# Performance work log

Measured on AMD Instinct MI355X. Metric: run time of the kernel, lower is better.

## Reference

```python
import jax, jax.numpy as jnp
import numpy as np

HEIGHT = 32
SIGMA = 2.0
NUM_NEGATIVE = 4096
N, C = 32, 512
L = HEIGHT * HEIGHT


def _grid_weight(height: int, sigma: float) -> jnp.ndarray:
    # distance_weights: pairwise Euclidean distance between grid points
    ii, jj = np.meshgrid(np.arange(height), np.arange(height), indexing='ij')
    coords = np.stack([ii.ravel(), jj.ravel()], axis=1).astype(np.float32)  # [L, 2]
    d2 = ((coords[:, None, :] - coords[None, :, :]) ** 2).sum(-1)  # squared dist [L, L]
    w = -(0.5 / sigma ** 2) * d2
    np.fill_diagonal(w, -np.inf)
    return jax.nn.softmax(jnp.asarray(w, dtype=jnp.float32), axis=1)


def setup_inputs() -> dict:
    key = jax.random.key(0)
    k1, k2 = jax.random.split(key)
    embedding = jax.random.normal(k1, (N, L, C), dtype=jnp.float32)
    weight = _grid_weight(HEIGHT, SIGMA)  # [L, L] softmax-normalized grid kernel
    neg_indices = jax.random.randint(k2, (NUM_NEGATIVE,), 0, N * L, dtype=jnp.int64)
    return {"embedding": embedding, "weight": weight, "neg_indices": neg_indices}


def reference(embedding, weight, neg_indices):
    n, l, c = embedding.shape
    # F.normalize(dim=-1), eps=1e-12
    norm = jnp.maximum(jnp.linalg.norm(embedding, axis=-1, keepdims=True), 1e-12)
    e = embedding / norm  # [N, L, C]
    # target = weight @ e  (broadcast over batch)
    target = jnp.einsum('kl,nlc->nkc', weight, e)  # [N, L, C]
    sim_pos = jnp.sum(e * target, axis=-1)  # [N, L]
    flat = e.reshape(-1, c)  # [N*L, C]
    negatives = flat[neg_indices]  # [M, C]
    sim_neg = jnp.einsum('nlc,mc->nlm', e, negatives)  # [N, L, M]
    logits = jnp.concatenate([sim_pos[..., None], sim_neg], axis=2).reshape(n * l, 1 + neg_indices.shape[0])
    # CrossEntropyLoss with target class 0, mean reduction
    loss = -jnp.mean(jax.nn.log_softmax(logits, axis=-1)[:, 0])
    return loss
```

## Files before the change

### kernel.cpp

```cpp
#include <hip/hip_runtime.h>
#include <hip/hip_bf16.h>
#include <stdint.h>

#define L_DIM 1024
#define C_DIM 512
#define CB4 256
#define N_BATCH 32
#define M_NEG 4096
#define NROWS (N_BATCH * L_DIM)

typedef float f32x4 __attribute__((ext_vector_type(4)));
typedef int i32x4 __attribute__((ext_vector_type(4)));
typedef int i32x8 __attribute__((ext_vector_type(8)));

#define E4_SCALE 32.0f
#define MX_SCALE 122
#define FMT_FP4 4

__device__ __forceinline__ void gl_lds16(const uint8_t* g, uint8_t* l) {
  __builtin_amdgcn_global_load_lds(
      (const __attribute__((address_space(1))) void*)g,
      (__attribute__((address_space(3))) void*)l, 16, 0, 0);
}

__device__ __forceinline__ uint32_t fp4_enc(float x) {
  const uint32_t s = (__float_as_uint(x) >> 31) << 3;
  const float a = fabsf(x);
  uint32_t c;
  c = a < 0.25f ? 0u
    : a < 0.75f ? 1u
    : a < 1.25f ? 2u
    : a < 1.75f ? 3u
    : a < 2.5f  ? 4u
    : a < 3.5f  ? 5u
    : a < 5.0f  ? 6u : 7u;
  return s | c;
}

__global__ __launch_bounds__(256) void k_normalize(const float* __restrict__ emb,
                                                   uint8_t* __restrict__ out,
                                                   float* __restrict__ zerobuf) {
  if (blockIdx.x < 256) zerobuf[blockIdx.x * 256 + threadIdx.x] = 0.0f;
  const int lane = threadIdx.x & 63;
  const int wave = threadIdx.x >> 6;
  const long row = (long)blockIdx.x * 4 + wave;
  const float4* src = (const float4*)(emb + row * C_DIM);
  float4 v0 = src[2 * lane];
  float4 v1 = src[2 * lane + 1];
  float ss = v0.x * v0.x + v0.y * v0.y + v0.z * v0.z + v0.w * v0.w +
             v1.x * v1.x + v1.y * v1.y + v1.z * v1.z + v1.w * v1.w;
#pragma unroll
  for (int off = 1; off < 64; off <<= 1) ss += __shfl_xor(ss, off, 64);
  const float s = E4_SCALE / fmaxf(sqrtf(ss), 1e-12f);
  uint32_t pk = fp4_enc(v0.x * s)        | (fp4_enc(v0.y * s) << 4) |
                (fp4_enc(v0.z * s) << 8) | (fp4_enc(v0.w * s) << 12) |
                (fp4_enc(v1.x * s) << 16)| (fp4_enc(v1.y * s) << 20) |
                (fp4_enc(v1.z * s) << 24)| (fp4_enc(v1.w * s) << 28);
  ((uint32_t*)(out + row * CB4))[lane] = pk;
}

__global__ __launch_bounds__(256, 2) void k_gemm_fused(
    const uint8_t* __restrict__ E4, const int* __restrict__ idx,
    const float* __restrict__ W, float* __restrict__ rowsum,
    float* __restrict__ simpos) {
  __shared__ __align__(16) unsigned char smem_raw[40960];
  uint8_t* sA = (uint8_t*)smem_raw;
  uint8_t* sB = sA + 256 * 64;

  const int tid = threadIdx.x;
  const int lane = tid & 63;
  const int wave = tid >> 6;
  const int wm = wave >> 1, wn = wave & 1;
  const int q = lane >> 4, c16 = lane & 15;

  const int bid = blockIdx.x;
  const bool is0 = bid >= 1024;
  long rowBase, colBase, n = 0;
  if (is0) {
    const int t = bid - 1024;
    const int xcd = t & 7, slot = t >> 3;
    rowBase = (long)(xcd * 16 + (slot & 15)) * 256;
    colBase = (long)(slot >> 4) * 128;
  } else {
    const int xcd = bid & 7, slot = bid >> 3;
    n = xcd * 4 + (slot & 3);
    const int inner = slot >> 2;
    rowBase = (long)(inner & 3) * 256;
    colBase = (long)(inner >> 2) * 128;
  }
  const long aBase = is0 ? rowBase : n * L_DIM + rowBase;

  long offA[4], offB[2];
#pragma unroll
  for (int r = 0; r < 4; ++r) {
    const int c = r * 256 + tid;
    const int rw = c >> 2, cb = c & 3;
    offA[r] = (aBase + rw) * CB4 + (cb ^ (rw & 3)) * 16;
  }
#pragma unroll
  for (int r = 0; r < 2; ++r) {
    const int c = r * 256 + tid;
    const int rw = c >> 2, cb = c & 3;
    const long bRow = is0 ? (long)idx[colBase + rw] : n * L_DIM + colBase + rw;
    offB[r] = bRow * CB4 + (cb ^ (rw & 3)) * 16;
  }

  f32x4 acc[8][4] = {};
  const i32x4 zz = {0, 0, 0, 0};

#pragma unroll
  for (int ks = 0; ks < CB4; ks += 64) {
#pragma unroll
    for (int r = 0; r < 4; ++r)
      gl_lds16(E4 + offA[r] + ks, sA + (r * 256 + tid) * 16);
#pragma unroll
    for (int r = 0; r < 2; ++r)
      gl_lds16(E4 + offB[r] + ks, sB + (r * 256 + tid) * 16);
    __syncthreads();
    i32x8 bfr[4];
#pragma unroll
    for (int j = 0; j < 4; ++j) {
      const int row = wn * 64 + j * 16 + c16;
      i32x4 d = *(const i32x4*)(sB + row * 64 + (q ^ (row & 3)) * 16);
      bfr[j] = __builtin_shufflevector(d, zz, 0, 1, 2, 3, 4, 5, 6, 7);
    }
#pragma unroll
    for (int i = 0; i < 8; ++i) {
      const int row = wm * 128 + i * 16 + c16;
      i32x4 d = *(const i32x4*)(sA + row * 64 + (q ^ (row & 3)) * 16);
      i32x8 af = __builtin_shufflevector(d, zz, 0, 1, 2, 3, 4, 5, 6, 7);
#pragma unroll
      for (int j = 0; j < 4; ++j)
        acc[i][j] = __builtin_amdgcn_mfma_scale_f32_16x16x128_f8f6f4(
            af, bfr[j], acc[i][j], FMT_FP4, FMT_FP4,
            0, MX_SCALE, 0, MX_SCALE);
    }
    __syncthreads();
  }

  if (is0) {
    float* S = (float*)smem_raw;
#pragma unroll
    for (int i = 0; i < 8; ++i)
#pragma unroll
      for (int r = 0; r < 4; ++r) {
        const float s = __expf(acc[i][0][r]) + __expf(acc[i][1][r]) +
                        __expf(acc[i][2][r]) + __expf(acc[i][3][r]);
        S[wave * 2560 + (i * 16 + q * 4 + r) * 20 + c16] = s;
      }
    __syncthreads();
    {
      const int wmg = tid >> 7, rs = tid & 127;
      const float4* p0 = (const float4*)(S + (wmg * 2 + 0) * 2560 + rs * 20);
      const float4* p1 = (const float4*)(S + (wmg * 2 + 1) * 2560 + rs * 20);
      float4 t0 = p0[0], t1 = p0[1], t2 = p0[2], t3 = p0[3];
      float4 u0 = p1[0], u1 = p1[1], u2 = p1[2], u3 = p1[3];
      float v = t0.x + t0.y + t0.z + t0.w + t1.x + t1.y + t1.z + t1.w +
                t2.x + t2.y + t2.z + t2.w + t3.x + t3.y + t3.z + t3.w +
                u0.x + u0.y + u0.z + u0.w + u1.x + u1.y + u1.z + u1.w +
                u2.x + u2.y + u2.z + u2.w + u3.x + u3.y + u3.z + u3.w;
      atomicAdd(&rowsum[rowBase + tid], v);
    }
  } else {
    float* G = (float*)smem_raw;
#pragma unroll
    for (int p = 0; p < 4; ++p) {
      if (wm == (p >> 1)) {
        const int ib = (p & 1) * 4;
#pragma unroll
        for (int ii = 0; ii < 4; ++ii)
#pragma unroll
          for (int j = 0; j < 4; ++j)
#pragma unroll
            for (int r = 0; r < 4; ++r)
              G[(ii * 16 + q * 4 + r) * 132 + wn * 64 + j * 16 + c16] =
                  acc[ib + ii][j][r];
      }
      __syncthreads();
      {
        const int rr = tid >> 2;
        const int chunk = tid & 3;
        const long krow = rowBase + p * 64 + rr;
        float v = 0.0f;
#pragma unroll
        for (int u = 0; u < 8; ++u) {
          const float4 g = *(const float4*)(G + rr * 132 + u * 16 + chunk * 4);
          const float4 w4 =
              *(const float4*)(W + krow * L_DIM + colBase + u * 16 + chunk * 4);
          v += g.x * w4.x + g.y * w4.y + g.z * w4.z + g.w * w4.w;
        }
        v += __shfl_xor(v, 1, 64);
        v += __shfl_xor(v, 2, 64);
        if (chunk == 0) atomicAdd(&simpos[n * L_DIM + krow], v);
      }
      __syncthreads();
    }
  }
}

__global__ __launch_bounds__(1024) void k_finalize(const float* __restrict__ rowsum,
                                                   const float* __restrict__ simpos,
                                                   float* __restrict__ out) {
  const int tid = threadIdx.x;
  float local = 0.0f;
  for (int r = tid; r < NROWS; r += 1024) {
    const float sp = simpos[r];
    local += logf(rowsum[r] + __expf(sp)) - sp;
  }
#pragma unroll
  for (int off = 1; off < 64; off <<= 1) local += __shfl_xor(local, off, 64);
  __shared__ float ws[16];
  if ((tid & 63) == 0) ws[tid >> 6] = local;
  __syncthreads();
  if (tid < 64) {
    float v = (tid < 16) ? ws[tid] : 0.0f;
#pragma unroll
    for (int off = 1; off < 16; off <<= 1) v += __shfl_xor(v, off, 64);
    if (tid == 0) out[0] = v * (1.0f / (float)NROWS);
  }
}

extern "C" void kernel_launch(void* const* d_in, const int* in_sizes, int n_in,
                              void* d_out, int out_size, void* d_ws, size_t ws_size,
                              hipStream_t stream) {
  const float* emb = (const float*)d_in[0];
  const float* weight = (const float*)d_in[1];
  const int* negidx = (const int*)d_in[2];
  float* out = (float*)d_out;
  char* ws = (char*)d_ws;

  uint8_t* E4 = (uint8_t*)ws;
  float* rowsum = (float*)(ws + 8388608);
  float* simpos = (float*)(ws + 8519680);

  k_normalize<<<NROWS / 4, 256, 0, stream>>>(emb, E4, rowsum);
  k_gemm_fused<<<5120, 256, 0, stream>>>(E4, negidx, weight, rowsum, simpos);
  k_finalize<<<1, 1024, 0, stream>>>(rowsum, simpos, out);
}
```

Before: 177.2 us.

## Load GEMM fragments directly from global memory and parallelize finalize reduction

The fused GEMM now loads FP4 MFMA operand fragments from global memory straight into registers instead of staging tiles through LDS with barriers. This removes LDS writes and reads and all syncthreads in the K loop, at the cost of redundant global reads across waves and strided, less coalesced access. The finalize kernel becomes a multi-block grid that reduces per block and atomically accumulates into the output, which is now zeroed in the normalize kernel. This replaces the single-block serial reduction.

```diff
diff --git a/kernel.cpp b/kernel.cpp
--- a/kernel.cpp
+++ b/kernel.cpp
@@ -16,12 +16,6 @@
 #define E4_SCALE 32.0f
 #define MX_SCALE 122
 #define FMT_FP4 4
-
-__device__ __forceinline__ void gl_lds16(const uint8_t* g, uint8_t* l) {
-  __builtin_amdgcn_global_load_lds(
-      (const __attribute__((address_space(1))) void*)g,
-      (__attribute__((address_space(3))) void*)l, 16, 0, 0);
-}
 
 __device__ __forceinline__ uint32_t fp4_enc(float x) {
   const uint32_t s = (__float_as_uint(x) >> 31) << 3;
@@ -39,8 +33,10 @@
 
 __global__ __launch_bounds__(256) void k_normalize(const float* __restrict__ emb,
                                                    uint8_t* __restrict__ out,
-                                                   float* __restrict__ zerobuf) {
+                                                   float* __restrict__ zerobuf,
+                                                   float* __restrict__ loss_out) {
   if (blockIdx.x < 256) zerobuf[blockIdx.x * 256 + threadIdx.x] = 0.0f;
+  if (blockIdx.x == 0 && threadIdx.x == 0) loss_out[0] = 0.0f;
   const int lane = threadIdx.x & 63;
   const int wave = threadIdx.x >> 6;
   const long row = (long)blockIdx.x * 4 + wave;
@@ -64,8 +60,6 @@
     const float* __restrict__ W, float* __restrict__ rowsum,
     float* __restrict__ simpos) {
   __shared__ __align__(16) unsigned char smem_raw[40960];
-  uint8_t* sA = (uint8_t*)smem_raw;
-  uint8_t* sB = sA + 256 * 64;
 
   const int tid = threadIdx.x;
   const int lane = tid & 63;
@@ -90,52 +84,42 @@
   }
   const long aBase = is0 ? rowBase : n * L_DIM + rowBase;
 
-  long offA[4], offB[2];
-#pragma unroll
-  for (int r = 0; r < 4; ++r) {
-    const int c = r * 256 + tid;
-    const int rw = c >> 2, cb = c & 3;
-    offA[r] = (aBase + rw) * CB4 + (cb ^ (rw & 3)) * 16;
-  }
-#pragma unroll
-  for (int r = 0; r < 2; ++r) {
-    const int c = r * 256 + tid;
-    const int rw = c >> 2, cb = c & 3;
-    const long bRow = is0 ? (long)idx[colBase + rw] : n * L_DIM + colBase + rw;
-    offB[r] = bRow * CB4 + (cb ^ (rw & 3)) * 16;
+  const uint8_t* aptr[8];
+#pragma unroll
+  for (int i = 0; i < 8; ++i)
+    aptr[i] = E4 + (aBase + wm * 128 + i * 16 + c16) * CB4 + q * 16;
+  const uint8_t* bptr[4];
+#pragma unroll
+  for (int j = 0; j < 4; ++j) {
+    const int brow = wn * 64 + j * 16 + c16;
+    const long bRow = is0 ? (long)idx[colBase + brow] : n * L_DIM + colBase + brow;
+    bptr[j] = E4 + bRow * CB4 + q * 16;
   }
 
   f32x4 acc[8][4] = {};
   const i32x4 zz = {0, 0, 0, 0};
 
 #pragma unroll
-  for (int ks = 0; ks < CB4; ks += 64) {
-#pragma unroll
-    for (int r = 0; r < 4; ++r)
-      gl_lds16(E4 + offA[r] + ks, sA + (r * 256 + tid) * 16);
-#pragma unroll
-    for (int r = 0; r < 2; ++r)
-      gl_lds16(E4 + offB[r] + ks, sB + (r * 256 + tid) * 16);
-    __syncthreads();
+  for (int ks = 0; ks < 4; ++ks) {
+    i32x4 a4[8];
+    i32x4 b4[4];
+#pragma unroll
+    for (int j = 0; j < 4; ++j) b4[j] = *(const i32x4*)(bptr[j] + ks * 64);
+#pragma unroll
+    for (int i = 0; i < 8; ++i) a4[i] = *(const i32x4*)(aptr[i] + ks * 64);
     i32x8 bfr[4];
 #pragma unroll
-    for (int j = 0; j < 4; ++j) {
-      const int row = wn * 64 + j * 16 + c16;
-      i32x4 d = *(const i32x4*)(sB + row * 64 + (q ^ (row & 3)) * 16);
-      bfr[j] = __builtin_shufflevector(d, zz, 0, 1, 2, 3, 4, 5, 6, 7);
-    }
+    for (int j = 0; j < 4; ++j)
+      bfr[j] = __builtin_shufflevector(b4[j], zz, 0, 1, 2, 3, 4, 5, 6, 7);
 #pragma unroll
     for (int i = 0; i < 8; ++i) {
-      const int row = wm * 128 + i * 16 + c16;
-      i32x4 d = *(const i32x4*)(sA + row * 64 + (q ^ (row & 3)) * 16);
-      i32x8 af = __builtin_shufflevector(d, zz, 0, 1, 2, 3, 4, 5, 6, 7);
+      i32x8 af = __builtin_shufflevector(a4[i], zz, 0, 1, 2, 3, 4, 5, 6, 7);
 #pragma unroll
       for (int j = 0; j < 4; ++j)
         acc[i][j] = __builtin_amdgcn_mfma_scale_f32_16x16x128_f8f6f4(
             af, bfr[j], acc[i][j], FMT_FP4, FMT_FP4,
             0, MX_SCALE, 0, MX_SCALE);
     }
-    __syncthreads();
   }
 
   if (is0) {
@@ -198,26 +182,19 @@
   }
 }
 
-__global__ __launch_bounds__(1024) void k_finalize(const float* __restrict__ rowsum,
-                                                   const float* __restrict__ simpos,
-                                                   float* __restrict__ out) {
-  const int tid = threadIdx.x;
-  float local = 0.0f;
-  for (int r = tid; r < NROWS; r += 1024) {
-    const float sp = simpos[r];
-    local += logf(rowsum[r] + __expf(sp)) - sp;
-  }
-#pragma unroll
-  for (int off = 1; off < 64; off <<= 1) local += __shfl_xor(local, off, 64);
-  __shared__ float ws[16];
-  if ((tid & 63) == 0) ws[tid >> 6] = local;
+__global__ __launch_bounds__(256) void k_finalize(const float* __restrict__ rowsum,
+                                                  const float* __restrict__ simpos,
+                                                  float* __restrict__ out) {
+  const int gid = blockIdx.x * 256 + threadIdx.x;
+  const float sp = simpos[gid];
+  float v = __logf(rowsum[gid] + __expf(sp)) - sp;
+#pragma unroll
+  for (int off = 1; off < 64; off <<= 1) v += __shfl_xor(v, off, 64);
+  __shared__ float ws[4];
+  if ((threadIdx.x & 63) == 0) ws[threadIdx.x >> 6] = v;
   __syncthreads();
-  if (tid < 64) {
-    float v = (tid < 16) ? ws[tid] : 0.0f;
-#pragma unroll
-    for (int off = 1; off < 16; off <<= 1) v += __shfl_xor(v, off, 64);
-    if (tid == 0) out[0] = v * (1.0f / (float)NROWS);
-  }
+  if (threadIdx.x == 0)
+    atomicAdd(out, (ws[0] + ws[1] + ws[2] + ws[3]) * (1.0f / (float)NROWS));
 }
 
 extern "C" void kernel_launch(void* const* d_in, const int* in_sizes, int n_in,
@@ -233,7 +210,7 @@
   float* rowsum = (float*)(ws + 8388608);
   float* simpos = (float*)(ws + 8519680);
 
-  k_normalize<<<NROWS / 4, 256, 0, stream>>>(emb, E4, rowsum);
+  k_normalize<<<NROWS / 4, 256, 0, stream>>>(emb, E4, rowsum, out);
   k_gemm_fused<<<5120, 256, 0, stream>>>(E4, negidx, weight, rowsum, simpos);
-  k_finalize<<<1, 1024, 0, stream>>>(rowsum, simpos, out);
-}
+  k_finalize<<<NROWS / 256, 256, 0, stream>>>(rowsum, simpos, out);
+}
```

New measurement: 234.8 us. +32.5%, slower.
